# Optimization experiments

Measured on AMD Instinct MI355X. Metric: run time of the kernel, lower is better.

Reference implementation:

```python
import jax, jax.numpy as jnp
import numpy as np

NH = 16
D = 1024
B, T = 4, 4096


def setup_inputs() -> dict:
    key = jax.random.key(0)
    k1, k2, k3, k4 = jax.random.split(key, 4)
    x = jax.random.normal(k1, (B, T, D), dtype=jnp.float32)
    phi = jax.random.normal(k2, (B, T), dtype=jnp.float32)
    W_attn = jax.random.normal(k3, (D, D), dtype=jnp.float32) * 0.02
    W_proj = jax.random.normal(k4, (D, D), dtype=jnp.float32) * 0.02
    gamma = jnp.ones((NH, 1), dtype=jnp.float32)
    temp = jnp.ones((NH, 1), dtype=jnp.float32)
    return {"x": x, "phi": phi, "W_attn": W_attn, "W_proj": W_proj,
            "gamma": gamma, "temp": temp}


def reference(x, phi, W_attn, W_proj, gamma, temp):
    Bb, Tt, d = x.shape
    hd = d // NH
    # c_attn (no bias), split heads: [B, nh, T, hd]
    w = (x @ W_attn.T).reshape(Bb, Tt, NH, hd).transpose(0, 2, 1, 3)
    w_sq = w * w
    denom = jnp.maximum(jnp.cumsum(w_sq, axis=-2), 1e-12)
    w_norm = w_sq / denom
    tssa_score = w_norm.sum(-1) * temp                       # [B, nh, T]
    phi_Q = phi[:, None, :]                                  # [B, 1, T]
    steps = jnp.arange(1, Tt + 1, dtype=x.dtype)
    mean_phi = jnp.cumsum(phi, axis=-1)[:, None, :] / steps  # running mean of phi
    penalty = (phi_Q - mean_phi) ** 2                        # [B, 1, T]
    score = tssa_score - gamma * penalty                     # [B, nh, T]
    alpha = jax.nn.softmax(score, axis=1)                    # softmax over HEADS (dim=1)
    dots = jnp.cumsum(w_sq * alpha[..., None], axis=-2) / (
        jnp.cumsum(alpha, axis=-1)[..., None] + 1e-8)
    attn = jnp.minimum(1.0 / (1.0 + dots), 10000.0)
    y = -w * alpha[..., None] * attn                          # [B, nh, T, hd]
    y = y.transpose(0, 2, 1, 3).reshape(Bb, Tt, d)
    y = y @ W_proj.T                                          # dropout is identity (p=0 / eval)
    return (y, alpha)
```

## Files before the change

### kernel.cpp

```cpp
#include <hip/hip_runtime.h>
#include <hip/hip_bf16.h>
#include <stdint.h>

#define NHh 16
#define Dm  1024
#define HD  64
#define Bb  4
#define Tt  4096
#define NCH 128
#define CHL 32

using bf16 = __hip_bfloat16;
typedef __attribute__((ext_vector_type(8))) short short8;
typedef __attribute__((ext_vector_type(4))) float f32x4;

__device__ __forceinline__ float bf2f(bf16 v) { return __bfloat162float(v); }

__device__ __forceinline__ float b2f(unsigned short u) {
  union { unsigned int i; float f; } x; x.i = ((unsigned int)u) << 16; return x.f;
}

__device__ __forceinline__ float frcp(float x) {
  float r; asm("v_rcp_f32 %0, %1" : "=v"(r) : "v"(x)); return r;
}

__device__ __forceinline__ void gld_lds16(const void* g, void* l) {
  __builtin_amdgcn_global_load_lds(
      (const __attribute__((address_space(1))) unsigned int*)g,
      (__attribute__((address_space(3))) unsigned int*)l, 16, 0, 0);
}

__global__ void cast_f32_to_bf16(const float* __restrict__ in, bf16* __restrict__ out, int n) {
  const int stride = gridDim.x * blockDim.x;
  for (int i = blockIdx.x * blockDim.x + threadIdx.x; i * 4 < n; i += stride) {
    const float4 v = *(const float4*)(in + (size_t)i * 4);
    ushort4 o;
    o.x = __bfloat16_as_ushort(__float2bfloat16(v.x));
    o.y = __bfloat16_as_ushort(__float2bfloat16(v.y));
    o.z = __bfloat16_as_ushort(__float2bfloat16(v.z));
    o.w = __bfloat16_as_ushort(__float2bfloat16(v.w));
    *(ushort4*)(out + (size_t)i * 4) = o;
  }
}

template <bool OUT_BF16, bool WRITE_S1>
__global__ __launch_bounds__(256) void gemm_bt(const bf16* __restrict__ A,
                                               const bf16* __restrict__ W,
                                               void* __restrict__ Cout,
                                               float* __restrict__ S1,
                                               int M, int N, int K) {
  __shared__ __align__(16) unsigned short sA[128][32];
  __shared__ __align__(16) unsigned short sB[128][32];
  const int tid  = threadIdx.x;
  const int lane = tid & 63;
  const int wave = tid >> 6;
  const int bid = blockIdx.x + blockIdx.y * gridDim.x;
  const int swz = ((bid & 7) << 7) | (bid >> 3);
  const int bn = (swz & 7) * 128;
  const int bm = (swz >> 3) * 128;
  const int wm = (wave & 1) * 64;
  const int wn = (wave >> 1) * 64;
  const int quad = lane >> 4;
  const int l16  = lane & 15;

  f32x4 acc[4][4] = {};

  const int rowL = tid >> 2;
  const int col8 = (tid & 3) * 8;

  for (int k0 = 0; k0 < K; k0 += 32) {
    const bf16* g0 = A + (size_t)(bm + rowL) * K + (k0 + col8);
    const bf16* g1 = A + (size_t)(bm + 64 + rowL) * K + (k0 + col8);
    gld_lds16(g0, (unsigned short*)sA + wave * 512);
    gld_lds16(g1, (unsigned short*)sA + 2048 + wave * 512);
    const bf16* h0 = W + (size_t)(bn + rowL) * K + (k0 + col8);
    const bf16* h1 = W + (size_t)(bn + 64 + rowL) * K + (k0 + col8);
    gld_lds16(h0, (unsigned short*)sB + wave * 512);
    gld_lds16(h1, (unsigned short*)sB + 2048 + wave * 512);
    __syncthreads();

    short8 af[4], bfv[4];
#pragma unroll
    for (int i = 0; i < 4; i++) af[i]  = *(const short8*)&sA[wm + i * 16 + l16][quad * 8];
#pragma unroll
    for (int j = 0; j < 4; j++) bfv[j] = *(const short8*)&sB[wn + j * 16 + l16][quad * 8];
#pragma unroll
    for (int i = 0; i < 4; i++)
#pragma unroll
      for (int j = 0; j < 4; j++)
        acc[i][j] = __builtin_amdgcn_mfma_f32_16x16x32_bf16(af[i], bfv[j], acc[i][j], 0, 0, 0);
    __syncthreads();
  }

#pragma unroll
  for (int j = 0; j < 4; j++) {
    const int col = bn + wn + j * 16 + l16;
    float ssum0 = 0.f, ssum1 = 0.f;
#pragma unroll
    for (int i = 0; i < 4; i++) {
#pragma unroll
      for (int r = 0; r < 4; r++) {
        const int row = bm + wm + i * 16 + quad * 4 + r;
        if constexpr (OUT_BF16) {
          const bf16 hv = __float2bfloat16(acc[i][j][r]);
          ((bf16*)Cout)[(size_t)row * N + col] = hv;
          if constexpr (WRITE_S1) {
            const float fv = bf2f(hv);
            if (i < 2) ssum0 += fv * fv; else ssum1 += fv * fv;
          }
        } else {
          ((float*)Cout)[(size_t)row * N + col] = acc[i][j][r];
        }
      }
    }
    if constexpr (WRITE_S1) {
      ssum0 += __shfl_xor(ssum0, 16, 64);
      ssum0 += __shfl_xor(ssum0, 32, 64);
      ssum1 += __shfl_xor(ssum1, 16, 64);
      ssum1 += __shfl_xor(ssum1, 32, 64);
      if (quad == 0) {
        const int r0 = bm + wm;
        const int b  = r0 >> 12;
        const int c0 = (r0 & (Tt - 1)) >> 5;
        const int h  = col >> 6, d = col & 63;
        float* s1p = S1 + (((size_t)(b * NHh + h) * NCH) + c0) * HD + d;
        s1p[0]  = ssum0;
        s1p[HD] = ssum1;
      }
    }
  }
}

__global__ __launch_bounds__(1024) void phi_penalty_kernel(const float* __restrict__ phi,
                                                           float* __restrict__ penalty) {
  const int b = blockIdx.x;
  const int tid = threadIdx.x;
  const int lane = tid & 63, wid = tid >> 6;
  __shared__ float wsum[16];
  __shared__ float carry_s;
  if (tid == 0) carry_s = 0.f;
  __syncthreads();
  for (int r = 0; r < Tt / 1024; r++) {
    const int t = r * 1024 + tid;
    const float v = phi[b * Tt + t];
    float incl = v;
#pragma unroll
    for (int off = 1; off < 64; off <<= 1) {
      float n = __shfl_up(incl, off, 64);
      if (lane >= off) incl += n;
    }
    if (lane == 63) wsum[wid] = incl;
    __syncthreads();
    float woff = carry_s;
    for (int wpre = 0; wpre < wid; wpre++) woff += wsum[wpre];
    const float csum = woff + incl;
    const float mean = csum / (float)(t + 1);
    const float dphi = v - mean;
    penalty[b * Tt + t] = dphi * dphi;
    __syncthreads();
    if (tid == 0) {
      float s = 0.f;
      for (int w = 0; w < 16; w++) s += wsum[w];
      carry_s += s;
    }
    __syncthreads();
  }
}

__global__ __launch_bounds__(64) void prefix_vec(float* __restrict__ S) {
  __shared__ float tile[NCH * HD];
  const int bh = blockIdx.x, tid = threadIdx.x;
  float* p = S + (size_t)bh * NCH * HD;
  const float4* src = (const float4*)p;
  float4* dst = (float4*)tile;
#pragma unroll 4
  for (int k = 0; k < (NCH * HD / 4) / 64; k++) dst[k * 64 + tid] = src[k * 64 + tid];
  __syncthreads();
  float run = 0.f;
  for (int c = 0; c < NCH; c++) {
    const float v = tile[c * HD + tid];
    tile[c * HD + tid] = run;
    run += v;
  }
  __syncthreads();
  float4* out = (float4*)p;
#pragma unroll 4
  for (int k = 0; k < (NCH * HD / 4) / 64; k++) out[k * 64 + tid] = dst[k * 64 + tid];
}

__global__ __launch_bounds__(64) void prefix_dots(float* __restrict__ S2, float* __restrict__ SA) {
  __shared__ float tile[NCH * HD];
  const int bh = blockIdx.x, tid = threadIdx.x;
  float* q = SA + (size_t)bh * NCH;
  const float v0 = q[tid], v1 = q[64 + tid];
  float i0 = v0;
#pragma unroll
  for (int off = 1; off < 64; off <<= 1) {
    const float n = __shfl_up(i0, off, 64);
    if (tid >= off) i0 += n;
  }
  const float tot0 = __shfl(i0, 63, 64);
  float i1 = v1;
#pragma unroll
  for (int off = 1; off < 64; off <<= 1) {
    const float n = __shfl_up(i1, off, 64);
    if (tid >= off) i1 += n;
  }
  i1 += tot0;
  q[tid] = i0 - v0;
  q[64 + tid] = i1 - v1;
  float* p = S2 + (size_t)bh * NCH * HD;
  const float4* src = (const float4*)p;
  float4* dst = (float4*)tile;
#pragma unroll 4
  for (int k = 0; k < (NCH * HD / 4) / 64; k++) dst[k * 64 + tid] = src[k * 64 + tid];
  __syncthreads();
  float run = 0.f;
  for (int c = 0; c < NCH; c++) {
    const float v = tile[c * HD + tid];
    tile[c * HD + tid] = run;
    run += v;
  }
  __syncthreads();
  float4* out = (float4*)p;
#pragma unroll 4
  for (int k = 0; k < (NCH * HD / 4) / 64; k++) out[k * 64 + tid] = dst[k * 64 + tid];
}

__global__ __launch_bounds__(64) void tssa_phase3(const bf16* __restrict__ w,
                                                  const float* __restrict__ Sex,
                                                  const float* __restrict__ temp,
                                                  float* __restrict__ tssa) {
  const int g = threadIdx.x >> 4, l = threadIdx.x & 15;
  const int c = blockIdx.x * 4 + g, h = blockIdx.y, b = blockIdx.z;
  const float4 ex = *(const float4*)&Sex[(((size_t)(b * NHh + h) * NCH) + c) * HD + l * 4];
  float a0 = ex.x, a1 = ex.y, a2 = ex.z, a3 = ex.w;
  const bf16* wp = w + ((size_t)(b * Tt + c * CHL)) * Dm + h * HD + l * 4;
  const float tv = temp[h];
  float* op = tssa + ((size_t)(b * Tt + c * CHL)) * NHh + h;
#pragma unroll 8
  for (int i = 0; i < CHL; i++) {
    const ushort4 v = *(const ushort4*)(wp + (size_t)i * Dm);
    const float f0 = b2f(v.x), f1 = b2f(v.y), f2 = b2f(v.z), f3 = b2f(v.w);
    const float s0 = f0 * f0, s1 = f1 * f1, s2 = f2 * f2, s3 = f3 * f3;
    a0 += s0; a1 += s1; a2 += s2; a3 += s3;
    float val = s0 * frcp(fmaxf(a0, 1e-12f)) + s1 * frcp(fmaxf(a1, 1e-12f))
              + s2 * frcp(fmaxf(a2, 1e-12f)) + s3 * frcp(fmaxf(a3, 1e-12f));
    val += __shfl_xor(val, 1, 64);
    val += __shfl_xor(val, 2, 64);
    val += __shfl_xor(val, 4, 64);
    val += __shfl_xor(val, 8, 64);
    if (l == 0) op[(size_t)i * NHh] = tv * val;
  }
}

__global__ void softmax_heads(const float* __restrict__ tssa, const float* __restrict__ penalty,
                              const float* __restrict__ gamma, float* __restrict__ alpha_f) {
  const int idx = blockIdx.x * blockDim.x + threadIdx.x;
  const int b = idx >> 12;
  const int t = idx & 4095;
  const float pen = penalty[idx];
  float sc[NHh];
  const float4* tp = (const float4*)(tssa + (size_t)idx * NHh);
#pragma unroll
  for (int q = 0; q < 4; q++) {
    const float4 v = tp[q];
    sc[q * 4 + 0] = v.x; sc[q * 4 + 1] = v.y; sc[q * 4 + 2] = v.z; sc[q * 4 + 3] = v.w;
  }
  float mx = -1e30f;
#pragma unroll
  for (int h = 0; h < NHh; h++) {
    sc[h] -= gamma[h] * pen;
    mx = fmaxf(mx, sc[h]);
  }
  float sum = 0.f;
#pragma unroll
  for (int h = 0; h < NHh; h++) { const float e = __expf(sc[h] - mx); sc[h] = e; sum += e; }
  const float inv = 1.f / sum;
#pragma unroll
  for (int h = 0; h < NHh; h++) {
    alpha_f[((size_t)(b * NHh + h)) * Tt + t] = sc[h] * inv;
  }
}

__global__ __launch_bounds__(64) void dots_phase1(const bf16* __restrict__ w,
                                                  const float* __restrict__ alpha_f,
                                                  float* __restrict__ S2, float* __restrict__ SA) {
  const int g = threadIdx.x >> 4, l = threadIdx.x & 15;
  const int c = blockIdx.x * 4 + g, h = blockIdx.y, b = blockIdx.z;
  const bf16* wp = w + ((size_t)(b * Tt + c * CHL)) * Dm + h * HD + l * 4;
  const float* ap = alpha_f + (size_t)(b * NHh + h) * Tt + c * CHL;
  float a0 = 0.f, a1 = 0.f, a2 = 0.f, a3 = 0.f, acca = 0.f;
#pragma unroll 8
  for (int i = 0; i < CHL; i++) {
    const float a = ap[i];
    const ushort4 v = *(const ushort4*)(wp + (size_t)i * Dm);
    const float f0 = b2f(v.x), f1 = b2f(v.y), f2 = b2f(v.z), f3 = b2f(v.w);
    a0 += f0 * f0 * a; a1 += f1 * f1 * a; a2 += f2 * f2 * a; a3 += f3 * f3 * a;
    acca += a;
  }
  float4 o; o.x = a0; o.y = a1; o.z = a2; o.w = a3;
  *(float4*)&S2[(((size_t)(b * NHh + h) * NCH) + c) * HD + l * 4] = o;
  if (l == 0) SA[(size_t)(b * NHh + h) * NCH + c] = acca;
}

__global__ __launch_bounds__(64) void y_phase3(const bf16* __restrict__ w,
                                               const float* __restrict__ alpha_f,
                                               const float* __restrict__ S2ex,
                                               const float* __restrict__ SAex,
                                               bf16* __restrict__ yprime) {
  const int g = threadIdx.x >> 4, l = threadIdx.x & 15;
  const int c = blockIdx.x * 4 + g, h = blockIdx.y, b = blockIdx.z;
  const float4 ex = *(const float4*)&S2ex[(((size_t)(b * NHh + h) * NCH) + c) * HD + l * 4];
  float a0 = ex.x, a1 = ex.y, a2 = ex.z, a3 = ex.w;
  float acca = SAex[(size_t)(b * NHh + h) * NCH + c];
  const bf16* wp = w + ((size_t)(b * Tt + c * CHL)) * Dm + h * HD + l * 4;
  const float* ap = alpha_f + (size_t)(b * NHh + h) * Tt + c * CHL;
  bf16* yp = yprime + ((size_t)(b * Tt + c * CHL)) * Dm + h * HD + l * 4;
#pragma unroll 8
  for (int i = 0; i < CHL; i++) {
    const float a = ap[i];
    const ushort4 v = *(const ushort4*)(wp + (size_t)i * Dm);
    const float f0 = b2f(v.x), f1 = b2f(v.y), f2 = b2f(v.z), f3 = b2f(v.w);
    a0 += f0 * f0 * a; a1 += f1 * f1 * a; a2 += f2 * f2 * a; a3 += f3 * f3 * a;
    acca += a;
    const float rinv = frcp(acca + 1e-8f);
    const float at0 = fminf(frcp(1.f + a0 * rinv), 10000.f);
    const float at1 = fminf(frcp(1.f + a1 * rinv), 10000.f);
    const float at2 = fminf(frcp(1.f + a2 * rinv), 10000.f);
    const float at3 = fminf(frcp(1.f + a3 * rinv), 10000.f);
    ushort4 o;
    o.x = __bfloat16_as_ushort(__float2bfloat16(-f0 * a * at0));
    o.y = __bfloat16_as_ushort(__float2bfloat16(-f1 * a * at1));
    o.z = __bfloat16_as_ushort(__float2bfloat16(-f2 * a * at2));
    o.w = __bfloat16_as_ushort(__float2bfloat16(-f3 * a * at3));
    *(ushort4*)(yp + (size_t)i * Dm) = o;
  }
}

extern "C" void kernel_launch(void* const* d_in, const int* in_sizes, int n_in,
                              void* d_out, int out_size, void* d_ws, size_t ws_size,
                              hipStream_t stream) {
  const float* x     = (const float*)d_in[0];
  const float* phi   = (const float*)d_in[1];
  const float* Wattn = (const float*)d_in[2];
  const float* Wproj = (const float*)d_in[3];
  const float* gamma = (const float*)d_in[4];
  const float* temp  = (const float*)d_in[5];

  float* y_out    = (float*)d_out;
  float* alpha_f  = y_out + (size_t)Bb * Tt * Dm;

  char* ws = (char*)d_ws;
  bf16*  x_bf   = (bf16*)ws;  ws += (size_t)Bb * Tt * Dm * 2;
  bf16*  Wa_bf  = (bf16*)ws;  ws += (size_t)Dm * Dm * 2;
  bf16*  Wp_bf  = (bf16*)ws;  ws += (size_t)Dm * Dm * 2;
  bf16*  w_bf   = (bf16*)ws;  ws += (size_t)Bb * Tt * Dm * 2;
  float* tssa   = (float*)ws; ws += (size_t)Bb * Tt * NHh * 4;
  float* pen    = (float*)ws; ws += (size_t)Bb * Tt * 4;
  float* S1     = (float*)ws; ws += (size_t)Bb * NHh * NCH * HD * 4;
  float* S2     = (float*)ws; ws += (size_t)Bb * NHh * NCH * HD * 4;
  float* SA     = (float*)ws; ws += (size_t)Bb * NHh * NCH * 4;
  bf16*  yprime = x_bf;

  const int M = Bb * Tt, N = Dm, K = Dm;
  dim3 gg(N / 128, M / 128), gb(256);
  dim3 g3(NCH / 4, NHh, Bb), b64(64);

  cast_f32_to_bf16<<<dim3(1024), dim3(256), 0, stream>>>(x, x_bf, Bb * Tt * Dm);
  cast_f32_to_bf16<<<dim3(256), dim3(256), 0, stream>>>(Wattn, Wa_bf, Dm * Dm);
  cast_f32_to_bf16<<<dim3(256), dim3(256), 0, stream>>>(Wproj, Wp_bf, Dm * Dm);

  gemm_bt<true, true><<<gg, gb, 0, stream>>>(x_bf, Wa_bf, (void*)w_bf, S1, M, N, K);
  phi_penalty_kernel<<<dim3(Bb), dim3(1024), 0, stream>>>(phi, pen);
  prefix_vec<<<dim3(Bb * NHh), b64, 0, stream>>>(S1);
  tssa_phase3<<<g3, b64, 0, stream>>>(w_bf, S1, temp, tssa);
  softmax_heads<<<dim3(Bb * Tt / 256), dim3(256), 0, stream>>>(tssa, pen, gamma, alpha_f);
  dots_phase1<<<g3, b64, 0, stream>>>(w_bf, alpha_f, S2, SA);
  prefix_dots<<<dim3(Bb * NHh), b64, 0, stream>>>(S2, SA);
  y_phase3<<<g3, b64, 0, stream>>>(w_bf, alpha_f, S2, SA, yprime);
  gemm_bt<false, false><<<gg, gb, 0, stream>>>(yprime, Wp_bf, (void*)y_out, nullptr, M, N, K);
}
```

Measured before the change: 289.6 us.

## Replace GEMM with 256x256 double-buffered swizzled-LDS tile kernel

Rewrites both GEMMs as a 512-thread kernel with 256x256x64 tiles, double-buffered LDS loads via global_load_lds, XOR-swizzled LDS layout to avoid bank conflicts, and prefetch of the next K-slice interleaved with MFMA work. The goal is more reuse per loaded byte, fewer barriers per FLOP, and load latency hidden behind compute. The fused S1 sum-of-squares epilogue is extended to four 32-row chunks per wave. It uses 128 KB of dynamic LDS per block and many accumulator registers, and the grid shrinks to 256 blocks, which could cost occupancy.

```diff
diff --git a/kernel.cpp b/kernel.cpp
--- a/kernel.cpp
+++ b/kernel.cpp
@@ -9,6 +9,11 @@
 #define Tt  4096
 #define NCH 128
 #define CHL 32
+
+#define BM 256
+#define BN 256
+#define BK 64
+#define NKT (Dm / BK)
 
 using bf16 = __hip_bfloat16;
 typedef __attribute__((ext_vector_type(8))) short short8;
@@ -44,91 +49,163 @@
 }
 
 template <bool OUT_BF16, bool WRITE_S1>
-__global__ __launch_bounds__(256) void gemm_bt(const bf16* __restrict__ A,
-                                               const bf16* __restrict__ W,
-                                               void* __restrict__ Cout,
-                                               float* __restrict__ S1,
-                                               int M, int N, int K) {
-  __shared__ __align__(16) unsigned short sA[128][32];
-  __shared__ __align__(16) unsigned short sB[128][32];
+__global__ __launch_bounds__(512, 2) void gemm256(const bf16* __restrict__ A,
+                                                  const bf16* __restrict__ W,
+                                                  void* __restrict__ Cout,
+                                                  float* __restrict__ S1,
+                                                  int M, int N, int K) {
+  extern __shared__ char smem[];
   const int tid  = threadIdx.x;
   const int lane = tid & 63;
   const int wave = tid >> 6;
-  const int bid = blockIdx.x + blockIdx.y * gridDim.x;
-  const int swz = ((bid & 7) << 7) | (bid >> 3);
-  const int bn = (swz & 7) * 128;
-  const int bm = (swz >> 3) * 128;
-  const int wm = (wave & 1) * 64;
-  const int wn = (wave >> 1) * 64;
+  const int bid = blockIdx.x;
+  const int swz = (bid & 7) * 32 + (bid >> 3);
+  const int bn = (swz & 3) * BN;
+  const int bm = (swz >> 2) * BM;
+  const int wm = (wave >> 2) * 128;
+  const int wn = (wave & 3) * 64;
   const int quad = lane >> 4;
   const int l16  = lane & 15;
 
-  f32x4 acc[4][4] = {};
-
-  const int rowL = tid >> 2;
-  const int col8 = (tid & 3) * 8;
-
-  for (int k0 = 0; k0 < K; k0 += 32) {
-    const bf16* g0 = A + (size_t)(bm + rowL) * K + (k0 + col8);
-    const bf16* g1 = A + (size_t)(bm + 64 + rowL) * K + (k0 + col8);
-    gld_lds16(g0, (unsigned short*)sA + wave * 512);
-    gld_lds16(g1, (unsigned short*)sA + 2048 + wave * 512);
-    const bf16* h0 = W + (size_t)(bn + rowL) * K + (k0 + col8);
-    const bf16* h1 = W + (size_t)(bn + 64 + rowL) * K + (k0 + col8);
-    gld_lds16(h0, (unsigned short*)sB + wave * 512);
-    gld_lds16(h1, (unsigned short*)sB + 2048 + wave * 512);
-    __syncthreads();
-
-    short8 af[4], bfv[4];
-#pragma unroll
-    for (int i = 0; i < 4; i++) af[i]  = *(const short8*)&sA[wm + i * 16 + l16][quad * 8];
-#pragma unroll
-    for (int j = 0; j < 4; j++) bfv[j] = *(const short8*)&sB[wn + j * 16 + l16][quad * 8];
-#pragma unroll
-    for (int i = 0; i < 4; i++)
-#pragma unroll
-      for (int j = 0; j < 4; j++)
-        acc[i][j] = __builtin_amdgcn_mfma_f32_16x16x32_bf16(af[i], bfv[j], acc[i][j], 0, 0, 0);
-    __syncthreads();
-  }
-
-#pragma unroll
-  for (int j = 0; j < 4; j++) {
-    const int col = bn + wn + j * 16 + l16;
-    float ssum0 = 0.f, ssum1 = 0.f;
-#pragma unroll
-    for (int i = 0; i < 4; i++) {
-#pragma unroll
-      for (int r = 0; r < 4; r++) {
-        const int row = bm + wm + i * 16 + quad * 4 + r;
-        if constexpr (OUT_BF16) {
-          const bf16 hv = __float2bfloat16(acc[i][j][r]);
+  const int srow = wave * 8 + (lane >> 3);
+  const int scol = (((lane & 7) ^ (lane >> 3)) << 3);
+
+  const bf16* Abase = A + (size_t)(bm + srow) * K + scol;
+  const bf16* Wbase = W + (size_t)(bn + srow) * K + scol;
+
+  f32x4 acc[8][4] = {};
+
+#define LDSA(buf, n) (smem + (buf) * 65536 + (n) * 8192 + wave * 1024)
+#define LDSB(buf, n) (smem + (buf) * 65536 + 32768 + (n) * 8192 + wave * 1024)
+
+#define STAGE_A(buf, n, k0) gld_lds16(Abase + (size_t)(n) * 64 * K + (k0), LDSA(buf, n))
+#define STAGE_B(buf, n, k0) gld_lds16(Wbase + (size_t)(n) * 64 * K + (k0), LDSB(buf, n))
+
+#define LD_FRAG(base, r, s) (*(const short8*)((base) + (size_t)(r) * 128 + ((((s) ^ ((r) & 7))) << 4)))
+
+#pragma unroll
+  for (int n = 0; n < 4; n++) STAGE_A(0, n, 0);
+#pragma unroll
+  for (int n = 0; n < 4; n++) STAGE_B(0, n, 0);
+  asm volatile("s_waitcnt vmcnt(0)" ::: "memory");
+  __builtin_amdgcn_s_barrier();
+  __builtin_amdgcn_sched_barrier(0);
+
+  for (int j = 0; j < NKT; j++) {
+    const int buf = j & 1;
+    const char* aL = smem + buf * 65536;
+    const char* bL = smem + buf * 65536 + 32768;
+    const int k0n = (j + 1) * BK;
+    const bool pf = (j + 1 < NKT);
+
+    short8 bfv[4][2];
+#pragma unroll
+    for (int nj = 0; nj < 4; nj++) {
+      const int r = wn + nj * 16 + l16;
+      bfv[nj][0] = LD_FRAG(bL, r, quad);
+      bfv[nj][1] = LD_FRAG(bL, r, quad + 4);
+    }
+    short8 af[4][2];
+#pragma unroll
+    for (int mi = 0; mi < 4; mi++) {
+      const int r = wm + mi * 16 + l16;
+      af[mi][0] = LD_FRAG(aL, r, quad);
+      af[mi][1] = LD_FRAG(aL, r, quad + 4);
+    }
+    if (pf) {
+      STAGE_A(buf ^ 1, 0, k0n); STAGE_A(buf ^ 1, 1, k0n);
+      STAGE_A(buf ^ 1, 2, k0n); STAGE_A(buf ^ 1, 3, k0n);
+    }
+    __builtin_amdgcn_s_setprio(1);
+#pragma unroll
+    for (int mi = 0; mi < 4; mi++)
+#pragma unroll
+      for (int nj = 0; nj < 4; nj++) {
+        acc[mi][nj] = __builtin_amdgcn_mfma_f32_16x16x32_bf16(af[mi][0], bfv[nj][0], acc[mi][nj], 0, 0, 0);
+        acc[mi][nj] = __builtin_amdgcn_mfma_f32_16x16x32_bf16(af[mi][1], bfv[nj][1], acc[mi][nj], 0, 0, 0);
+      }
+    __builtin_amdgcn_s_setprio(0);
+    __builtin_amdgcn_sched_barrier(0);
+
+#pragma unroll
+    for (int mi = 0; mi < 4; mi++) {
+      const int r = wm + 64 + mi * 16 + l16;
+      af[mi][0] = LD_FRAG(aL, r, quad);
+      af[mi][1] = LD_FRAG(aL, r, quad + 4);
+    }
+    if (pf) {
+      STAGE_B(buf ^ 1, 0, k0n); STAGE_B(buf ^ 1, 1, k0n);
+      STAGE_B(buf ^ 1, 2, k0n); STAGE_B(buf ^ 1, 3, k0n);
+    }
+    __builtin_amdgcn_s_setprio(1);
+#pragma unroll
+    for (int mi = 0; mi < 4; mi++)
+#pragma unroll
+      for (int nj = 0; nj < 4; nj++) {
+        acc[mi + 4][nj] = __builtin_amdgcn_mfma_f32_16x16x32_bf16(af[mi][0], bfv[nj][0], acc[mi + 4][nj], 0, 0, 0);
+        acc[mi + 4][nj] = __builtin_amdgcn_mfma_f32_16x16x32_bf16(af[mi][1], bfv[nj][1], acc[mi + 4][nj], 0, 0, 0);
+      }
+    __builtin_amdgcn_s_setprio(0);
+
+    asm volatile("s_waitcnt vmcnt(0)" ::: "memory");
+    __builtin_amdgcn_s_barrier();
+    __builtin_amdgcn_sched_barrier(0);
+  }
+
+#pragma unroll
+  for (int nj = 0; nj < 4; nj++) {
+    const int col = bn + wn + nj * 16 + l16;
+    if constexpr (OUT_BF16) {
+      float ss0 = 0.f, ss1 = 0.f, ss2 = 0.f, ss3 = 0.f;
+#pragma unroll
+      for (int mi = 0; mi < 8; mi++) {
+        float csum = 0.f;
+#pragma unroll
+        for (int r = 0; r < 4; r++) {
+          const int row = bm + wm + mi * 16 + quad * 4 + r;
+          const bf16 hv = __float2bfloat16(acc[mi][nj][r]);
           ((bf16*)Cout)[(size_t)row * N + col] = hv;
-          if constexpr (WRITE_S1) {
-            const float fv = bf2f(hv);
-            if (i < 2) ssum0 += fv * fv; else ssum1 += fv * fv;
-          }
-        } else {
-          ((float*)Cout)[(size_t)row * N + col] = acc[i][j][r];
+          if constexpr (WRITE_S1) { const float fv = bf2f(hv); csum += fv * fv; }
+        }
+        if constexpr (WRITE_S1) {
+          if (mi < 2) ss0 += csum;
+          else if (mi < 4) ss1 += csum;
+          else if (mi < 6) ss2 += csum;
+          else ss3 += csum;
         }
       }
-    }
-    if constexpr (WRITE_S1) {
-      ssum0 += __shfl_xor(ssum0, 16, 64);
-      ssum0 += __shfl_xor(ssum0, 32, 64);
-      ssum1 += __shfl_xor(ssum1, 16, 64);
-      ssum1 += __shfl_xor(ssum1, 32, 64);
-      if (quad == 0) {
-        const int r0 = bm + wm;
-        const int b  = r0 >> 12;
-        const int c0 = (r0 & (Tt - 1)) >> 5;
-        const int h  = col >> 6, d = col & 63;
-        float* s1p = S1 + (((size_t)(b * NHh + h) * NCH) + c0) * HD + d;
-        s1p[0]  = ssum0;
-        s1p[HD] = ssum1;
+      if constexpr (WRITE_S1) {
+        ss0 += __shfl_xor(ss0, 16, 64); ss0 += __shfl_xor(ss0, 32, 64);
+        ss1 += __shfl_xor(ss1, 16, 64); ss1 += __shfl_xor(ss1, 32, 64);
+        ss2 += __shfl_xor(ss2, 16, 64); ss2 += __shfl_xor(ss2, 32, 64);
+        ss3 += __shfl_xor(ss3, 16, 64); ss3 += __shfl_xor(ss3, 32, 64);
+        if (quad == 0) {
+          const int h = col >> 6, d = col & 63;
+          const int r0 = bm + wm;
+          const int b  = r0 >> 12;
+          const int c0 = (r0 & (Tt - 1)) >> 5;
+          float* s1p = S1 + (((size_t)(b * NHh + h) * NCH) + c0) * HD + d;
+          s1p[0]      = ss0;
+          s1p[HD]     = ss1;
+          s1p[2 * HD] = ss2;
+          s1p[3 * HD] = ss3;
+        }
       }
-    }
-  }
+    } else {
+#pragma unroll
+      for (int mi = 0; mi < 8; mi++)
+#pragma unroll
+        for (int r = 0; r < 4; r++) {
+          const int row = bm + wm + mi * 16 + quad * 4 + r;
+          ((float*)Cout)[(size_t)row * N + col] = acc[mi][nj][r];
+        }
+    }
+  }
+#undef LDSA
+#undef LDSB
+#undef STAGE_A
+#undef STAGE_B
+#undef LD_FRAG
 }
 
 __global__ __launch_bounds__(1024) void phi_penalty_kernel(const float* __restrict__ phi,
@@ -363,15 +440,24 @@
   float* SA     = (float*)ws; ws += (size_t)Bb * NHh * NCH * 4;
   bf16*  yprime = x_bf;
 
+  static int attr_done = 0;
+  if (!attr_done) {
+    hipFuncSetAttribute((const void*)gemm256<true, true>,
+                        hipFuncAttributeMaxDynamicSharedMemorySize, 131072);
+    hipFuncSetAttribute((const void*)gemm256<false, false>,
+                        hipFuncAttributeMaxDynamicSharedMemorySize, 131072);
+    attr_done = 1;
+  }
+
   const int M = Bb * Tt, N = Dm, K = Dm;
-  dim3 gg(N / 128, M / 128), gb(256);
+  dim3 gg((M / BM) * (N / BN)), gb(512);
   dim3 g3(NCH / 4, NHh, Bb), b64(64);
 
   cast_f32_to_bf16<<<dim3(1024), dim3(256), 0, stream>>>(x, x_bf, Bb * Tt * Dm);
   cast_f32_to_bf16<<<dim3(256), dim3(256), 0, stream>>>(Wattn, Wa_bf, Dm * Dm);
   cast_f32_to_bf16<<<dim3(256), dim3(256), 0, stream>>>(Wproj, Wp_bf, Dm * Dm);
 
-  gemm_bt<true, true><<<gg, gb, 0, stream>>>(x_bf, Wa_bf, (void*)w_bf, S1, M, N, K);
+  gemm256<true, true><<<gg, gb, 131072, stream>>>(x_bf, Wa_bf, (void*)w_bf, S1, M, N, K);
   phi_penalty_kernel<<<dim3(Bb), dim3(1024), 0, stream>>>(phi, pen);
   prefix_vec<<<dim3(Bb * NHh), b64, 0, stream>>>(S1);
   tssa_phase3<<<g3, b64, 0, stream>>>(w_bf, S1, temp, tssa);
@@ -379,5 +465,5 @@
   dots_phase1<<<g3, b64, 0, stream>>>(w_bf, alpha_f, S2, SA);
   prefix_dots<<<dim3(Bb * NHh), b64, 0, stream>>>(S2, SA);
   y_phase3<<<g3, b64, 0, stream>>>(w_bf, alpha_f, S2, SA, yprime);
-  gemm_bt<false, false><<<gg, gb, 0, stream>>>(yprime, Wp_bf, (void*)y_out, nullptr, M, N, K);
-}
+  gemm256<false, false><<<gg, gb, 131072, stream>>>(yprime, Wp_bf, (void*)y_out, nullptr, M, N, K);
+}
```

After: 264.0 us. 1.1x faster.
